# Kernel tuning notes

Hardware: AMD Instinct MI355X
Metric: run time of the kernel (lower is better)

## Reference

```python
import jax, jax.numpy as jnp
import numpy as np

K = 3          # kernel size
PAD = 1        # padding
# deformable conv v2: offset conv (2*K*K ch), modulator conv (K*K ch, 2*sigmoid), main 3x3 conv, ReLU


def _conv2d(x, w, b):
    y = jax.lax.conv_general_dilated(x, w, (1, 1), ((PAD, PAD), (PAD, PAD)),
                                     dimension_numbers=('NCHW', 'OIHW', 'NCHW'))
    return y + b[None, :, None, None]


def _bilinear_gather(x, py, px):
    # x: [B,C,H,W]; py/px: [B,K2,H,W] float sample coords; zero outside image.
    B, C, H, W = x.shape
    y0 = jnp.floor(py)
    x0 = jnp.floor(px)
    wy1 = py - y0
    wx1 = px - x0
    wy0 = 1.0 - wy1
    wx0 = 1.0 - wx1
    xf = x.reshape(B, C, H * W)

    def gather(yi, xi):
        valid = (yi >= 0) & (yi <= H - 1) & (xi >= 0) & (xi <= W - 1)
        yc = jnp.clip(yi, 0, H - 1).astype(jnp.int32)
        xc = jnp.clip(xi, 0, W - 1).astype(jnp.int32)
        idx = (yc * W + xc).reshape(B, -1)                      # [B, K2*H*W]
        v = jax.vmap(lambda xb, ib: xb[:, ib])(xf, idx)         # [B, C, K2*H*W]
        v = v.reshape(B, C, *yi.shape[1:])                      # [B, C, K2, H, W]
        return v * valid[:, None].astype(x.dtype)

    return (gather(y0, x0) * (wy0 * wx0)[:, None]
            + gather(y0, x0 + 1) * (wy0 * wx1)[:, None]
            + gather(y0 + 1, x0) * (wy1 * wx0)[:, None]
            + gather(y0 + 1, x0 + 1) * (wy1 * wx1)[:, None])


def _deform_conv(data, w, b, w_off, b_off, w_mod, b_mod):
    B, Cin, H, W = data.shape
    off = _conv2d(data, w_off, b_off)                           # [B, 2*K2, H, W]
    mask = 2.0 * jax.nn.sigmoid(_conv2d(data, w_mod, b_mod))    # [B, K2, H, W]
    off = off.reshape(B, K * K, 2, H, W)                        # (dy, dx) per tap
    dy, dx = off[:, :, 0], off[:, :, 1]
    ki, kj = jnp.meshgrid(jnp.arange(K), jnp.arange(K), indexing='ij')
    ki = ki.reshape(-1).astype(data.dtype)
    kj = kj.reshape(-1).astype(data.dtype)
    hs = jnp.arange(H, dtype=data.dtype)
    ws = jnp.arange(W, dtype=data.dtype)
    py = hs[None, None, :, None] - PAD + ki[None, :, None, None] + dy
    px = ws[None, None, None, :] - PAD + kj[None, :, None, None] + dx
    sampled = _bilinear_gather(data, py, px)                    # [B, Cin, K2, H, W]
    sampled = sampled * mask[:, None]
    out = jnp.einsum('bckhw,ock->bohw', sampled, w.reshape(w.shape[0], Cin, K * K))
    return out + b[None, :, None, None]


def setup_inputs() -> dict:
    key = jax.random.key(0)
    ks = jax.random.split(key, 7)
    B, Cin, Cout, H, W = 8, 64, 64, 128, 128
    fan = Cin * K * K
    return {
        'data': jax.random.normal(ks[0], (B, Cin, H, W), jnp.float32),
        'w': jax.random.normal(ks[1], (Cout, Cin, K, K), jnp.float32) / np.sqrt(fan),
        'b': jax.random.normal(ks[2], (Cout,), jnp.float32) * 0.01,
        'w_off': jax.random.normal(ks[3], (2 * K * K, Cin, K, K), jnp.float32) * (0.1 / np.sqrt(fan)),
        'b_off': jnp.zeros((2 * K * K,), jnp.float32),
        'w_mod': jax.random.normal(ks[4], (K * K, Cin, K, K), jnp.float32) * (0.1 / np.sqrt(fan)),
        'b_mod': jnp.zeros((K * K,), jnp.float32),
    }


def reference(data, w, b, w_off, b_off, w_mod, b_mod):
    return jax.nn.relu(_deform_conv(data, w, b, w_off, b_off, w_mod, b_mod))
```

## Files before the change

kernel.cpp:

```cpp
#include <hip/hip_runtime.h>
#include <cstdint>


typedef __attribute__((ext_vector_type(8))) short short8;
typedef __attribute__((ext_vector_type(4))) float floatx4;

__device__ __forceinline__ unsigned short f2bf(float x) {
    unsigned int u = __float_as_uint(x);
    u += 0x7fffu + ((u >> 16) & 1u);
    return (unsigned short)(u >> 16);
}
__device__ __forceinline__ float bflo(unsigned int u) { return __uint_as_float(u << 16); }
__device__ __forceinline__ float bfhi(unsigned int u) { return __uint_as_float(u & 0xffff0000u); }
__device__ __forceinline__ unsigned int pack2bf(float lo, float hi) {
    unsigned int ul = __float_as_uint(lo); ul += 0x7fffu + ((ul >> 16) & 1u);
    unsigned int uh = __float_as_uint(hi); uh += 0x7fffu + ((uh >> 16) & 1u);
    return __builtin_amdgcn_perm(uh, ul, 0x07060302u);
}
__device__ __forceinline__ unsigned int blend2(unsigned int a, unsigned int b,
                                               unsigned int c, unsigned int d,
                                               float4 fw) {
    float lo = fw.x * bflo(a) + fw.y * bflo(b) + fw.z * bflo(c) + fw.w * bflo(d);
    float hi = fw.x * bfhi(a) + fw.y * bfhi(b) + fw.z * bfhi(c) + fw.w * bfhi(d);
    return pack2bf(lo, hi);
}

#define OFF_DATAT 0u
#define OFF_OFFP  16777216u
#define OFF_WM    30932992u
#define OFF_W27   31006720u
#define OFF_B27   31043584u

__global__ void pack_weights_k(const float* __restrict__ w,
                               const float* __restrict__ w_off,
                               const float* __restrict__ w_mod,
                               const float* __restrict__ b_off,
                               const float* __restrict__ b_mod,
                               unsigned short* __restrict__ wpackM,
                               unsigned short* __restrict__ wpack27,
                               float* __restrict__ bias27) {
    int t = blockIdx.x * 256 + threadIdx.x;
    if (t < 64 * 576) {
        int o = t / 576, kk = t % 576;
        int k = kk >> 6, c = kk & 63;
        wpackM[t] = f2bf(w[(o * 64 + c) * 9 + k]);
        return;
    }
    t -= 64 * 576;
    if (t < 32 * 576) {
        int o = t / 576, kk = t % 576;
        int k = kk >> 6, c = kk & 63;
        float v = 0.f;
        if (o < 18)      v = w_off[(o * 64 + c) * 9 + k];
        else if (o < 27) v = w_mod[((o - 18) * 64 + c) * 9 + k];
        wpack27[t] = f2bf(v);
        if (kk == 0) bias27[o] = (o < 18) ? b_off[o] : (o < 27 ? b_mod[o - 18] : 0.f);
    }
}

__global__ __launch_bounds__(256) void transpose_k(const float* __restrict__ x,
                                                   unsigned short* __restrict__ xt) {
    __shared__ float tile[64][65];
    int blk  = blockIdx.x;
    int b    = blk >> 8;
    int pos0 = (blk & 255) << 6;
    int lane = threadIdx.x & 63;
    int g    = threadIdx.x >> 6;
    for (int c = g; c < 64; c += 4)
        tile[c][lane] = x[(((b << 6) + c) << 14) + pos0 + lane];
    __syncthreads();
    int c2 = lane & 31;
    for (int i = g; i < 32; i += 4) {
        int pr = (i << 1) + (lane >> 5);
        unsigned int d = pack2bf(tile[c2 << 1][pr], tile[(c2 << 1) + 1][pr]);
        *(unsigned int*)&xt[((size_t)((b << 14) + pos0 + pr) << 6) + (c2 << 1)] = d;
    }
}

__global__ __launch_bounds__(256) void conv27_k(const unsigned short* __restrict__ xt,
                                                const unsigned short* __restrict__ wpack27,
                                                const float* __restrict__ bias27,
                                                float* __restrict__ offP) {
    __shared__ unsigned short tile[4][66][72];
    int blk   = blockIdx.x;
    int b     = blk >> 7;
    int patch = blk & 127;
    int m     = patch >> 1;
    int h     = patch & 1;
    int tid   = threadIdx.x;
    int lane  = tid & 63, wv = tid >> 6;
    int r = lane & 15, q = lane >> 4;

    const unsigned short* xb = xt + ((size_t)b << 20);

    {
        int g = tid >> 3, j = tid & 7;
        #pragma unroll
        for (int rr = 0; rr < 4; ++rr) {
            int sy = (m << 1) + rr - 1;
            #pragma unroll
            for (int ci = 0; ci < 3; ++ci) {
                int col = g + (ci << 5);
                if (col < 66) {
                    int sx = (h << 6) + col - 1;
                    uint4 v = {0u, 0u, 0u, 0u};
                    if (sy >= 0 && sy < 128 && sx >= 0 && sx < 128)
                        v = *(const uint4*)&xb[(size_t)(((sy << 7) + sx) << 6) + (j << 3)];
                    *(uint4*)&tile[rr][col][j << 3] = v;
                }
            }
        }
    }
    __syncthreads();

    floatx4 acc[4] = {};
    #pragma unroll
    for (int k = 0; k < 9; ++k) {
        int ki = k / 3, kj = k % 3;
        #pragma unroll
        for (int ch = 0; ch < 2; ++ch) {
            short8 a0 = *(const short8*)&wpack27[(r)      * 576 + (k << 6) + (ch << 5) + (q << 3)];
            short8 a1 = *(const short8*)&wpack27[(16 + r) * 576 + (k << 6) + (ch << 5) + (q << 3)];
            #pragma unroll
            for (int tr = 0; tr < 2; ++tr) {
                short8 bfrag = *(const short8*)&tile[tr + ki][(wv << 4) + r + kj][(ch << 5) + (q << 3)];
                acc[0 + tr] = __builtin_amdgcn_mfma_f32_16x16x32_bf16(a0, bfrag, acc[0 + tr], 0, 0, 0);
                acc[2 + tr] = __builtin_amdgcn_mfma_f32_16x16x32_bf16(a1, bfrag, acc[2 + tr], 0, 0, 0);
            }
        }
    }

    #pragma unroll
    for (int s = 0; s < 2; ++s) {
        #pragma unroll
        for (int tr = 0; tr < 2; ++tr) {
            #pragma unroll
            for (int reg = 0; reg < 4; ++reg) {
                int oc = (s << 4) + (q << 2) + reg;
                if (oc >= 27) continue;
                int pos = (((m << 1) + tr) << 7) + (h << 6) + (wv << 4) + r;
                float v = acc[(s << 1) + tr][reg] + bias27[oc];
                int kk, comp;
                if (oc < 18) { kk = oc >> 1; comp = oc & 1; }
                else         { kk = oc - 18; comp = 2; v = 2.f / (1.f + __expf(-v)); }
                offP[(size_t)(((b * 9 + kk) * 3 + comp) << 14) + pos] = v;
            }
        }
    }
}

__global__ __launch_bounds__(256) void deform_main_k(const unsigned short* __restrict__ xt,
                                                     const unsigned short* __restrict__ wpackM,
                                                     const float* __restrict__ offP,
                                                     const float* __restrict__ bias,
                                                     float* __restrict__ out) {
    __shared__ int4   pOff[576];
    __shared__ float4 pW[576];
    __shared__ unsigned short samp[64][72];
    int blk  = blockIdx.x;
    int b    = blk >> 8;
    int pos0 = (blk & 255) << 6;
    int tid  = threadIdx.x;
    int lane = tid & 63, wv = tid >> 6;
    int r = lane & 15, q = lane >> 4;
    int pg = lane >> 3;
    int j8 = lane & 7;

    const char* xbb = (const char*)(xt + ((size_t)b << 20));

    for (int e = tid; e < 576; e += 256) {
        int k = e >> 6, p = e & 63;
        int pos = pos0 + p;
        const float* offk = offP + ((size_t)((b * 9 + k) * 3) << 14);
        float dy = offk[pos];
        float dx = offk[16384 + pos];
        float m  = offk[32768 + pos];
        float py = (float)(pos >> 7) + (float)(k / 3 - 1) + dy;
        float px = (float)(pos & 127) + (float)(k % 3 - 1) + dx;
        float y0f = floorf(py), x0f = floorf(px);
        int y0 = (int)y0f, x0 = (int)x0f;
        float wy1 = py - y0f, wx1 = px - x0f;
        float wy0 = 1.f - wy1, wx0 = 1.f - wx1;
        bool vy0 = (y0 >= 0) && (y0 < 128);
        bool vy1 = (y0 >= -1) && (y0 < 127);
        bool vx0 = (x0 >= 0) && (x0 < 128);
        bool vx1 = (x0 >= -1) && (x0 < 127);
        float w00 = (vy0 && vx0) ? m * wy0 * wx0 : 0.f;
        float w01 = (vy0 && vx1) ? m * wy0 * wx1 : 0.f;
        float w10 = (vy1 && vx0) ? m * wy1 * wx0 : 0.f;
        float w11 = (vy1 && vx1) ? m * wy1 * wx1 : 0.f;
        int y0c = min(max(y0, 0), 127), y1c = min(max(y0 + 1, 0), 127);
        int x0c = min(max(x0, 0), 127), x1c = min(max(x0 + 1, 0), 127);
        pOff[e] = make_int4(((y0c << 7) + x0c) << 7, ((y0c << 7) + x1c) << 7,
                            ((y1c << 7) + x0c) << 7, ((y1c << 7) + x1c) << 7);
        pW[e] = make_float4(w00, w01, w10, w11);
    }

    floatx4 acc[4] = {};
    const char* xp = xbb + (j8 << 4);

    for (int k = 0; k < 9; ++k) {
        __syncthreads();
        #pragma unroll
        for (int i = 0; i < 2; ++i) {
            int p = (wv << 4) + (i << 3) + pg;
            int e = (k << 6) + p;
            int4   io = pOff[e];
            float4 fw = pW[e];
            uint4 u00 = *(const uint4*)(xp + io.x);
            uint4 u01 = *(const uint4*)(xp + io.y);
            uint4 u10 = *(const uint4*)(xp + io.z);
            uint4 u11 = *(const uint4*)(xp + io.w);
            uint4 o4;
            o4.x = blend2(u00.x, u01.x, u10.x, u11.x, fw);
            o4.y = blend2(u00.y, u01.y, u10.y, u11.y, fw);
            o4.z = blend2(u00.z, u01.z, u10.z, u11.z, fw);
            o4.w = blend2(u00.w, u01.w, u10.w, u11.w, fw);
            *(uint4*)&samp[p][j8 << 3] = o4;
        }
        __syncthreads();
        #pragma unroll
        for (int ch = 0; ch < 2; ++ch) {
            short8 afrag = *(const short8*)&wpackM[((wv << 4) + r) * 576 + (k << 6) + (ch << 5) + (q << 3)];
            #pragma unroll
            for (int nt = 0; nt < 4; ++nt) {
                short8 bfrag = *(const short8*)&samp[(nt << 4) + r][(ch << 5) + (q << 3)];
                acc[nt] = __builtin_amdgcn_mfma_f32_16x16x32_bf16(afrag, bfrag, acc[nt], 0, 0, 0);
            }
        }
    }

    #pragma unroll
    for (int nt = 0; nt < 4; ++nt) {
        #pragma unroll
        for (int reg = 0; reg < 4; ++reg) {
            int oc  = (wv << 4) + (q << 2) + reg;
            int pos = pos0 + (nt << 4) + r;
            float v = acc[nt][reg] + bias[oc];
            out[(size_t)(((b << 6) + oc) << 14) + pos] = fmaxf(v, 0.f);
        }
    }
}

extern "C" void kernel_launch(void* const* d_in, const int* in_sizes, int n_in,
                              void* d_out, int out_size, void* d_ws, size_t ws_size,
                              hipStream_t stream) {
    const float* data  = (const float*)d_in[0];
    const float* w     = (const float*)d_in[1];
    const float* bias  = (const float*)d_in[2];
    const float* w_off = (const float*)d_in[3];
    const float* b_off = (const float*)d_in[4];
    const float* w_mod = (const float*)d_in[5];
    const float* b_mod = (const float*)d_in[6];
    float* out = (float*)d_out;

    char* ws = (char*)d_ws;
    unsigned short* dataT   = (unsigned short*)(ws + OFF_DATAT);
    float*          offP    = (float*)(ws + OFF_OFFP);
    unsigned short* wpackM  = (unsigned short*)(ws + OFF_WM);
    unsigned short* wpack27 = (unsigned short*)(ws + OFF_W27);
    float*          bias27  = (float*)(ws + OFF_B27);

    pack_weights_k<<<216, 256, 0, stream>>>(w, w_off, w_mod, b_off, b_mod,
                                            wpackM, wpack27, bias27);
    transpose_k<<<2048, 256, 0, stream>>>(data, dataT);
    conv27_k<<<1024, 256, 0, stream>>>(dataT, wpack27, bias27, offP);
    deform_main_k<<<2048, 256, 0, stream>>>(dataT, wpackM, offP, bias, out);
}
```

Measured before the change: 172.5 us.

## Double-buffer deformable sample tile and prefetch next tap's gathers during MFMA

The main deformable conv kernel now double-buffers the shared-memory sample tile. It issues the global gathers and weight-fragment loads for tap k+1 before running the MFMAs for tap k, so gather latency overlaps matrix compute and one barrier per tap is dropped. The bilinear blend is also rewritten with packed float2 arithmetic and the HIP bf16x2 round conversion. In exchange it doubles the sample-tile LDS footprint and holds more prefetched data in registers, which may lower occupancy.

```diff
diff --git a/kernel.cpp b/kernel.cpp
--- a/kernel.cpp
+++ b/kernel.cpp
@@ -1,28 +1,37 @@
 #include <hip/hip_runtime.h>
+#include <hip/hip_bf16.h>
 #include <cstdint>
 
 
 typedef __attribute__((ext_vector_type(8))) short short8;
 typedef __attribute__((ext_vector_type(4))) float floatx4;
+typedef __attribute__((ext_vector_type(2))) float floatx2;
 
 __device__ __forceinline__ unsigned short f2bf(float x) {
     unsigned int u = __float_as_uint(x);
     u += 0x7fffu + ((u >> 16) & 1u);
     return (unsigned short)(u >> 16);
 }
-__device__ __forceinline__ float bflo(unsigned int u) { return __uint_as_float(u << 16); }
-__device__ __forceinline__ float bfhi(unsigned int u) { return __uint_as_float(u & 0xffff0000u); }
 __device__ __forceinline__ unsigned int pack2bf(float lo, float hi) {
     unsigned int ul = __float_as_uint(lo); ul += 0x7fffu + ((ul >> 16) & 1u);
     unsigned int uh = __float_as_uint(hi); uh += 0x7fffu + ((uh >> 16) & 1u);
     return __builtin_amdgcn_perm(uh, ul, 0x07060302u);
 }
-__device__ __forceinline__ unsigned int blend2(unsigned int a, unsigned int b,
-                                               unsigned int c, unsigned int d,
-                                               float4 fw) {
-    float lo = fw.x * bflo(a) + fw.y * bflo(b) + fw.z * bflo(c) + fw.w * bflo(d);
-    float hi = fw.x * bfhi(a) + fw.y * bfhi(b) + fw.z * bfhi(c) + fw.w * bfhi(d);
-    return pack2bf(lo, hi);
+__device__ __forceinline__ floatx2 up2(unsigned int u) {
+    floatx2 r;
+    r.x = __uint_as_float(u << 16);
+    r.y = __uint_as_float(u & 0xffff0000u);
+    return r;
+}
+__device__ __forceinline__ unsigned int blend2pk(unsigned int a, unsigned int b,
+                                                 unsigned int c, unsigned int d,
+                                                 float4 fw) {
+    floatx2 s = up2(a) * fw.x;
+    s += up2(b) * fw.y;
+    s += up2(c) * fw.z;
+    s += up2(d) * fw.w;
+    __hip_bfloat162 h = __float22bfloat162_rn(make_float2(s.x, s.y));
+    return *(unsigned int*)&h;
 }
 
 #define OFF_DATAT 0u
@@ -156,7 +165,7 @@
                                                      float* __restrict__ out) {
     __shared__ int4   pOff[576];
     __shared__ float4 pW[576];
-    __shared__ unsigned short samp[64][72];
+    __shared__ unsigned short samp[2][64][72];
     int blk  = blockIdx.x;
     int b    = blk >> 8;
     int pos0 = (blk & 255) << 6;
@@ -195,38 +204,65 @@
                             ((y1c << 7) + x0c) << 7, ((y1c << 7) + x1c) << 7);
         pW[e] = make_float4(w00, w01, w10, w11);
     }
+    __syncthreads();
 
     floatx4 acc[4] = {};
     const char* xp = xbb + (j8 << 4);
-
-    for (int k = 0; k < 9; ++k) {
-        __syncthreads();
+    const unsigned short* wrow = wpackM + ((wv << 4) + r) * 576 + (q << 3);
+
+    uint4  c00[2], c01[2], c10[2], c11[2];
+    float4 cw[2];
+    short8 afC[2], afN[2];
+
+    auto issue = [&](int k) {
+        #pragma unroll
+        for (int i = 0; i < 2; ++i) {
+            int e  = (k << 6) + (wv << 4) + (i << 3) + pg;
+            int4   io = pOff[e];
+            cw[i]  = pW[e];
+            c00[i] = *(const uint4*)(xp + io.x);
+            c01[i] = *(const uint4*)(xp + io.y);
+            c10[i] = *(const uint4*)(xp + io.z);
+            c11[i] = *(const uint4*)(xp + io.w);
+        }
+    };
+    auto blendStore = [&](int buf) {
         #pragma unroll
         for (int i = 0; i < 2; ++i) {
             int p = (wv << 4) + (i << 3) + pg;
-            int e = (k << 6) + p;
-            int4   io = pOff[e];
-            float4 fw = pW[e];
-            uint4 u00 = *(const uint4*)(xp + io.x);
-            uint4 u01 = *(const uint4*)(xp + io.y);
-            uint4 u10 = *(const uint4*)(xp + io.z);
-            uint4 u11 = *(const uint4*)(xp + io.w);
             uint4 o4;
-            o4.x = blend2(u00.x, u01.x, u10.x, u11.x, fw);
-            o4.y = blend2(u00.y, u01.y, u10.y, u11.y, fw);
-            o4.z = blend2(u00.z, u01.z, u10.z, u11.z, fw);
-            o4.w = blend2(u00.w, u01.w, u10.w, u11.w, fw);
-            *(uint4*)&samp[p][j8 << 3] = o4;
+            o4.x = blend2pk(c00[i].x, c01[i].x, c10[i].x, c11[i].x, cw[i]);
+            o4.y = blend2pk(c00[i].y, c01[i].y, c10[i].y, c11[i].y, cw[i]);
+            o4.z = blend2pk(c00[i].z, c01[i].z, c10[i].z, c11[i].z, cw[i]);
+            o4.w = blend2pk(c00[i].w, c01[i].w, c10[i].w, c11[i].w, cw[i]);
+            *(uint4*)&samp[buf][p][j8 << 3] = o4;
+        }
+    };
+
+    issue(0);
+    afC[0] = *(const short8*)&wrow[0];
+    afC[1] = *(const short8*)&wrow[32];
+    blendStore(0);
+
+    for (int k = 0; k < 9; ++k) {
+        if (k < 8) {
+            issue(k + 1);
+            afN[0] = *(const short8*)&wrow[((k + 1) << 6)];
+            afN[1] = *(const short8*)&wrow[((k + 1) << 6) + 32];
         }
         __syncthreads();
         #pragma unroll
         for (int ch = 0; ch < 2; ++ch) {
-            short8 afrag = *(const short8*)&wpackM[((wv << 4) + r) * 576 + (k << 6) + (ch << 5) + (q << 3)];
             #pragma unroll
             for (int nt = 0; nt < 4; ++nt) {
-                short8 bfrag = *(const short8*)&samp[(nt << 4) + r][(ch << 5) + (q << 3)];
-                acc[nt] = __builtin_amdgcn_mfma_f32_16x16x32_bf16(afrag, bfrag, acc[nt], 0, 0, 0);
+                short8 bfrag = *(const short8*)&samp[k & 1][(nt << 4) + r][(ch << 5) + (q << 3)];
+                acc[nt] = __builtin_amdgcn_mfma_f32_16x16x32_bf16(afC[ch], bfrag, acc[nt], 0, 0, 0);
             }
+        }
+        if (k < 8) {
+            blendStore((k + 1) & 1);
+            afC[0] = afN[0];
+            afC[1] = afN[1];
         }
     }
 
```

New measurement: 165.1 us. -4.3%, faster.
